# Kernel optimization log

Measured on AMD Instinct MI355X. Metric: run time of the kernel, lower is better.

## Reference

```python
import jax, jax.numpy as jnp
import numpy as np
import math

B, NTOK, NH, D = 8, 1000, 8, 64
CHUNK = 8  # query-chunk size for the pairwise L1 score computation


def _linearm(w, x):
    # LinearM: w [out, in+1] (last column is bias); x [b, t, in] -> [b, t, out]
    return jnp.einsum('oi,bti->bto', w[:, :-1], x) + w[:, -1]


def setup_inputs() -> dict:
    key = jax.random.key(0)
    ks = jax.random.split(key, 4)
    scl = 0.005
    x = jax.random.normal(ks[0], (B, NTOK, D), dtype=jnp.float32)
    wq = (scl * jax.random.normal(ks[1], (NH * D, D + 1), dtype=jnp.float32)).at[:, -1].set(0.0)
    wv = (scl * jax.random.normal(ks[2], (NH * D, D + 1), dtype=jnp.float32)).at[:, -1].set(0.0)
    wk = scl * jnp.ones((NH, D), dtype=jnp.float32)
    wf = (scl * jax.random.normal(ks[3], (D, D + 1), dtype=jnp.float32)).at[:, -1].set(0.0)
    return {"x": x, "wq": wq, "wv": wv, "wk": wk, "wf": wf}


def _forward(x, wq, wv, wk, wf):
    b, t, d = x.shape
    nh = wk.shape[0]
    scale = 1.0 / math.sqrt(d)

    q = _linearm(wq, x).reshape(b, t, nh, d)          # [b, t, nh, d]
    v = _linearm(wv, x).reshape(b, t, nh, d)          # [b, t, nh, d]
    k = x[:, :, None, :] * wk[None, None]             # [b, t, nh, d]

    # L1-distance attention scores: a[b, s, q, h] = -scale * sum_w |q[b,q,h,w] - k[b,s,h,w]|
    # Computed in query chunks so the [b, t, t, nh, d] pairwise tensor is never materialized.
    nc = t // CHUNK
    qc = q.reshape(b, nc, CHUNK, nh, d).transpose(1, 0, 2, 3, 4)  # [nc, b, C, nh, d]

    @jax.checkpoint
    def scores(qch):
        # qch: [b, C, nh, d] -> [b, t(src), C, nh]
        return -scale * jnp.sum(jnp.abs(qch[:, None] - k[:, :, None]), axis=-1)

    a = jax.lax.map(scores, qc)                       # [nc, b, t, C, nh]
    a = a.transpose(1, 2, 0, 3, 4).reshape(b, t, t, nh)  # [b, src, dst, nh]

    # Extra all-zero "null" source row (mirrors a[:, a2len, :, :] = 0 before softmax)
    a = jnp.concatenate([a, jnp.zeros((b, 1, t, nh), a.dtype)], axis=1)
    a = jax.nn.softmax(a, axis=1)[:, :t]              # softmax over sources, drop null row

    # einsum('bsdh,bshw->bdhw') followed by sum over heads, fused:
    out = jnp.einsum('bsth,bshw->btw', a, v)          # [b, t, d]

    y = jax.nn.relu(out)                              # self.gelu is actually ReLU
    y = _linearm(wf, y)
    return x + y


def reference(x, wq, wv, wk, wf):
    return _forward(x, wq, wv, wk, wf)
```

## Files before the change

kernel.cpp:

```cpp
#include <hip/hip_runtime.h>
#include <math.h>

#define Bb 8
#define Tt 1000
#define TPAD 1024
#define NHh 8
#define Dd 64

typedef short bf16x8 __attribute__((ext_vector_type(8)));
typedef float f32x4 __attribute__((ext_vector_type(4)));

#define QOFF (-0.3f)
#define QSTEP (0.6f / 256.0f)
#define QINV (256.0f / 0.6f)
#define CQ (-0.125f * 1.44269504088896341f * QSTEP)

__device__ __forceinline__ unsigned sad_u8(unsigned a, unsigned b, unsigned c) {
#if __has_builtin(__builtin_amdgcn_sad_u8)
    return __builtin_amdgcn_sad_u8(a, b, c);
#else
    unsigned d;
    asm("v_sad_u8 %0, %1, %2, %3" : "=v"(d) : "v"(a), "v"(b), "v"(c));
    return d;
#endif
}

__device__ __forceinline__ unsigned quant8(float v) {
    float t = (v - QOFF) * QINV + 0.5f;
    t = fminf(fmaxf(t, 0.0f), 255.0f);
    return (unsigned)(int)t;
}

__device__ __forceinline__ unsigned cvt_pk_bf16(float lo, float hi) {
    unsigned r;
    asm("v_cvt_pk_bf16_f32 %0, %1, %2" : "=v"(r) : "v"(lo), "v"(hi));
    return r;
}

__device__ __forceinline__ unsigned short f2bf(float v) {
    return (unsigned short)(cvt_pk_bf16(v, v) & 0xffffu);
}

__device__ __forceinline__ float bf2f(unsigned short u) {
    union { unsigned u; float f; } x; x.u = ((unsigned)u) << 16; return x.f;
}

__device__ __forceinline__ bf16x8 mkbf(unsigned u0, unsigned u1, unsigned u2, unsigned u3) {
    union { unsigned u[4]; bf16x8 v; } x;
    x.u[0] = u0; x.u[1] = u1; x.u[2] = u2; x.u[3] = u3;
    return x.v;
}

__device__ __forceinline__ bf16x8 bfc(uint4 q) {
    union { uint4 q; bf16x8 v; } x; x.q = q; return x.v;
}

#define GLDS(gsrc, ldst) \
    __builtin_amdgcn_global_load_lds((const __attribute__((address_space(1))) unsigned*)(gsrc), \
                                     (__attribute__((address_space(3))) unsigned*)(ldst), 16, 0, 0)

__global__ __launch_bounds__(256) void prep_kernel(
    const float* __restrict__ x, const float* __restrict__ wq,
    const float* __restrict__ wv, const float* __restrict__ wk,
    unsigned* __restrict__ qq8, unsigned* __restrict__ kq8,
    uint4* __restrict__ vfrag)
{
    __shared__ float xs[64][68];
    __shared__ float ws[64][65];
    __shared__ float vS[64][68];
    const int tid = threadIdx.x;
    const int st = blockIdx.x;
    const int cb = blockIdx.y;
    const int b  = blockIdx.z;
    const bool isQ = (cb < 8);
    const int h = isQ ? cb : (cb - 8);
    const float* W = isQ ? wq : wv;
    const int cBase = h * 64;
    const int bh = b * NHh + h;

#pragma unroll
    for (int i = 0; i < 4; ++i) {
        int f4 = tid + i * 256;
        int r = f4 >> 4, c4 = (f4 & 15) << 2;
        int row = st * 64 + r; if (row >= Tt) row = Tt - 1;
        *(float4*)&xs[r][c4] = *(const float4*)&x[((size_t)b * Tt + row) * 64 + c4];
    }
#pragma unroll
    for (int i = 0; i < 16; ++i) {
        int idx = tid + i * 256;
        int c = idx >> 6, k = idx & 63;
        ws[c][k] = W[(cBase + c) * 65 + k];
    }
    __syncthreads();

    const int rg = tid >> 4, cg = tid & 15;
    const int r0 = rg * 4, c0 = cg * 4;
    float acc[4][4];
#pragma unroll
    for (int j = 0; j < 4; ++j) {
        float bias = W[(cBase + c0 + j) * 65 + 64];
#pragma unroll
        for (int i = 0; i < 4; ++i) acc[i][j] = bias;
    }
    for (int k0 = 0; k0 < 64; k0 += 4) {
        float4 a[4];
#pragma unroll
        for (int i = 0; i < 4; ++i) a[i] = *(const float4*)&xs[r0 + i][k0];
#pragma unroll
        for (int j = 0; j < 4; ++j) {
            float b0 = ws[c0 + j][k0 + 0];
            float b1 = ws[c0 + j][k0 + 1];
            float b2 = ws[c0 + j][k0 + 2];
            float b3 = ws[c0 + j][k0 + 3];
#pragma unroll
            for (int i = 0; i < 4; ++i)
                acc[i][j] += a[i].x * b0 + a[i].y * b1 + a[i].z * b2 + a[i].w * b3;
        }
    }

    if (isQ) {
#pragma unroll
        for (int i = 0; i < 4; ++i) {
            int t = st * 64 + r0 + i;
            unsigned d = 0u;
            if (t < Tt)
                d = quant8(acc[i][0]) | (quant8(acc[i][1]) << 8) |
                    (quant8(acc[i][2]) << 16) | (quant8(acc[i][3]) << 24);
            qq8[((size_t)bh * TPAD + t) * 16 + cg] = d;
        }
        {
            const int r = tid >> 2, c4 = tid & 3;
            const int t = st * 64 + r;
            unsigned kd[4];
            if (t < Tt) {
#pragma unroll
                for (int dw = 0; dw < 4; ++dw) {
                    int w = c4 * 16 + dw * 4;
                    float4 wkv = *(const float4*)&wk[h * 64 + w];
                    kd[dw] = quant8(xs[r][w + 0] * wkv.x) |
                             (quant8(xs[r][w + 1] * wkv.y) << 8) |
                             (quant8(xs[r][w + 2] * wkv.z) << 16) |
                             (quant8(xs[r][w + 3] * wkv.w) << 24);
                }
            } else {
                kd[0] = kd[1] = kd[2] = kd[3] = 0u;
            }
            const int c4s = c4 ^ ((r >> 3) & 3);
            *(uint4*)&kq8[((size_t)bh * TPAD + t) * 16 + c4s * 4] =
                make_uint4(kd[0], kd[1], kd[2], kd[3]);
        }
    } else {
#pragma unroll
        for (int i = 0; i < 4; ++i) {
            float4 o; o.x = acc[i][0]; o.y = acc[i][1]; o.z = acc[i][2]; o.w = acc[i][3];
            *(float4*)&vS[r0 + i][c0] = o;
        }
        __syncthreads();
#pragma unroll
        for (int e2 = 0; e2 < 2; ++e2) {
            int ent = tid + e2 * 256;
            int kk = ent >> 8, rem = ent & 255, n = rem >> 6, lane = rem & 63;
            int ts = kk * 32 + ((lane >> 4) << 3);
            int w  = n * 16 + (lane & 15);
            unsigned o[4];
#pragma unroll
            for (int pr = 0; pr < 4; ++pr) {
                int t0 = st * 64 + ts + pr * 2;
                float lo = (t0 < Tt)     ? vS[ts + pr * 2][w]     : 0.0f;
                float hi = (t0 + 1 < Tt) ? vS[ts + pr * 2 + 1][w] : 0.0f;
                o[pr] = cvt_pk_bf16(lo, hi);
            }
            vfrag[(((size_t)bh * 16 + st) * 8 + (kk * 4 + n)) * 64 + lane] =
                make_uint4(o[0], o[1], o[2], o[3]);
        }
    }
}

__global__ __launch_bounds__(256) void attn_kernel(
    const unsigned* __restrict__ qq8, const unsigned* __restrict__ kq8,
    const uint4* __restrict__ vfrag,
    unsigned short* __restrict__ numbf, float* __restrict__ dsums)
{
    __shared__ uint4 smem[1024];
    __shared__ float dred[2][2][16];

    const int tid = threadIdx.x;
    const int wv_ = tid >> 6;
    const int l   = tid & 63;
    const int g   = l >> 4;
    const int m   = l & 15;
    const int qt  = blockIdx.x;
    const int h   = blockIdx.y;
    const int bz  = blockIdx.z;
    const int b   = bz >> 1;
    const int half = bz & 1;
    const int bh  = b * NHh + h;
    const int rowhalf = wv_ & 1;
    const int tileq   = wv_ >> 1;
    const int rowbase = qt * 64 + rowhalf * 32;
    const int tbase   = half * 8 + tileq * 4;

    unsigned qa[16], qb[16];
    {
        const uint4* qp = (const uint4*)qq8 + ((size_t)bh * TPAD + rowbase + m) * 4;
        *(uint4*)&qa[0]  = qp[0];  *(uint4*)&qa[4]  = qp[1];
        *(uint4*)&qa[8]  = qp[2];  *(uint4*)&qa[12] = qp[3];
        const uint4* qp2 = qp + 64;
        *(uint4*)&qb[0]  = qp2[0]; *(uint4*)&qb[4]  = qp2[1];
        *(uint4*)&qb[8]  = qp2[2]; *(uint4*)&qb[12] = qp2[3];
    }

    const uint4* kg = (const uint4*)kq8 + (size_t)bh * 4096;
    const uint4* vg = vfrag + (size_t)bh * 8192;

#define STAGEK(I, BUF) do { \
        GLDS(kg + (half * 8 + (I)) * 256 + wv_ * 64 + l,     &smem[(0 * 2 + (BUF)) * 256 + wv_ * 64]); \
        GLDS(kg + (half * 8 + 4 + (I)) * 256 + wv_ * 64 + l, &smem[(1 * 2 + (BUF)) * 256 + wv_ * 64]); \
    } while (0)

    STAGEK(0, 0);
    __syncthreads();

    f32x4 aca[4], acb[4];
#pragma unroll
    for (int n = 0; n < 4; ++n) { aca[n] = (f32x4){0.f,0.f,0.f,0.f}; acb[n] = aca[n]; }
    float dsum_a = 0.0f, dsum_b = 0.0f;

#pragma unroll 1
    for (int i = 0; i < 4; ++i) {
        const int cur = i & 1;
        const int t = tbase + i;
        const uint4* kbase = &smem[(tileq * 2 + cur) * 256];
        const uint4* vt = vg + (size_t)t * 512 + l;

        if (i < 3) STAGEK(i + 1, cur ^ 1);

        uint4 vf0 = vt[0 * 64], vf1 = vt[1 * 64], vf2 = vt[2 * 64], vf3 = vt[3 * 64];

        bf16x8 Aa0, Ab0;
        {
            unsigned wa[4], wb[4];
            float pva = 0.f, pvb = 0.f;
#pragma unroll
            for (int e = 0; e < 8; ++e) {
                const uint4* kb = kbase + ((g << 3) + e) * 4;
                uint4 c0 = kb[0 ^ g], c1 = kb[1 ^ g], c2 = kb[2 ^ g], c3 = kb[3 ^ g];
                const unsigned* k0 = (const unsigned*)&c0;
                const unsigned* k1 = (const unsigned*)&c1;
                const unsigned* k2 = (const unsigned*)&c2;
                const unsigned* k3 = (const unsigned*)&c3;
                unsigned sa0 = 0u, sa1 = 0u, sb0 = 0u, sb1 = 0u;
#pragma unroll
                for (int w = 0; w < 4; ++w) {
                    sa0 = sad_u8(qa[w],      k0[w], sa0);
                    sa1 = sad_u8(qa[4 + w],  k1[w], sa1);
                    sb0 = sad_u8(qb[w],      k0[w], sb0);
                    sb1 = sad_u8(qb[4 + w],  k1[w], sb1);
                }
#pragma unroll
                for (int w = 0; w < 4; ++w) {
                    sa0 = sad_u8(qa[8 + w],  k2[w], sa0);
                    sa1 = sad_u8(qa[12 + w], k3[w], sa1);
                    sb0 = sad_u8(qb[8 + w],  k2[w], sb0);
                    sb1 = sad_u8(qb[12 + w], k3[w], sb1);
                }
                float pea = __builtin_amdgcn_exp2f(CQ * (float)(sa0 + sa1));
                float peb = __builtin_amdgcn_exp2f(CQ * (float)(sb0 + sb1));
                dsum_a += pea; dsum_b += peb;
                if (e & 1) { wa[e >> 1] = cvt_pk_bf16(pva, pea); wb[e >> 1] = cvt_pk_bf16(pvb, peb); }
                else       { pva = pea; pvb = peb; }
            }
            Aa0 = mkbf(wa[0], wa[1], wa[2], wa[3]);
            Ab0 = mkbf(wb[0], wb[1], wb[2], wb[3]);
        }

        aca[0] = __builtin_amdgcn_mfma_f32_16x16x32_bf16(Aa0, bfc(vf0), aca[0], 0, 0, 0);
        acb[0] = __builtin_amdgcn_mfma_f32_16x16x32_bf16(Ab0, bfc(vf0), acb[0], 0, 0, 0);
        aca[1] = __builtin_amdgcn_mfma_f32_16x16x32_bf16(Aa0, bfc(vf1), aca[1], 0, 0, 0);
        acb[1] = __builtin_amdgcn_mfma_f32_16x16x32_bf16(Ab0, bfc(vf1), acb[1], 0, 0, 0);
        aca[2] = __builtin_amdgcn_mfma_f32_16x16x32_bf16(Aa0, bfc(vf2), aca[2], 0, 0, 0);
        acb[2] = __builtin_amdgcn_mfma_f32_16x16x32_bf16(Ab0, bfc(vf2), acb[2], 0, 0, 0);
        aca[3] = __builtin_amdgcn_mfma_f32_16x16x32_bf16(Aa0, bfc(vf3), aca[3], 0, 0, 0);
        acb[3] = __builtin_amdgcn_mfma_f32_16x16x32_bf16(Ab0, bfc(vf3), acb[3], 0, 0, 0);

        uint4 vf4 = vt[4 * 64], vf5 = vt[5 * 64], vf6 = vt[6 * 64], vf7 = vt[7 * 64];

        bf16x8 Aa1, Ab1;
        {
            const bool maskall = (t == 15) && (g >= 1);
            unsigned wa[4], wb[4];
            float pva = 0.f, pvb = 0.f;
#pragma unroll
            for (int e = 0; e < 8; ++e) {
                const uint4* kb = kbase + (32 + (g << 3) + e) * 4;
                uint4 c0 = kb[0 ^ g], c1 = kb[1 ^ g], c2 = kb[2 ^ g], c3 = kb[3 ^ g];
                const unsigned* k0 = (const unsigned*)&c0;
                const unsigned* k1 = (const unsigned*)&c1;
                const unsigned* k2 = (const unsigned*)&c2;
                const unsigned* k3 = (const unsigned*)&c3;
                unsigned sa0 = 0u, sa1 = 0u, sb0 = 0u, sb1 = 0u;
#pragma unroll
                for (int w = 0; w < 4; ++w) {
                    sa0 = sad_u8(qa[w],      k0[w], sa0);
                    sa1 = sad_u8(qa[4 + w],  k1[w], sa1);
                    sb0 = sad_u8(qb[w],      k0[w], sb0);
                    sb1 = sad_u8(qb[4 + w],  k1[w], sb1);
                }
#pragma unroll
                for (int w = 0; w < 4; ++w) {
                    sa0 = sad_u8(qa[8 + w],  k2[w], sa0);
                    sa1 = sad_u8(qa[12 + w], k3[w], sa1);
                    sb0 = sad_u8(qb[8 + w],  k2[w], sb0);
                    sb1 = sad_u8(qb[12 + w], k3[w], sb1);
                }
                float pea = maskall ? 0.0f : __builtin_amdgcn_exp2f(CQ * (float)(sa0 + sa1));
                float peb = maskall ? 0.0f : __builtin_amdgcn_exp2f(CQ * (float)(sb0 + sb1));
                dsum_a += pea; dsum_b += peb;
                if (e & 1) { wa[e >> 1] = cvt_pk_bf16(pva, pea); wb[e >> 1] = cvt_pk_bf16(pvb, peb); }
                else       { pva = pea; pvb = peb; }
            }
            Aa1 = mkbf(wa[0], wa[1], wa[2], wa[3]);
            Ab1 = mkbf(wb[0], wb[1], wb[2], wb[3]);
        }

        aca[0] = __builtin_amdgcn_mfma_f32_16x16x32_bf16(Aa1, bfc(vf4), aca[0], 0, 0, 0);
        acb[0] = __builtin_amdgcn_mfma_f32_16x16x32_bf16(Ab1, bfc(vf4), acb[0], 0, 0, 0);
        aca[1] = __builtin_amdgcn_mfma_f32_16x16x32_bf16(Aa1, bfc(vf5), aca[1], 0, 0, 0);
        acb[1] = __builtin_amdgcn_mfma_f32_16x16x32_bf16(Ab1, bfc(vf5), acb[1], 0, 0, 0);
        aca[2] = __builtin_amdgcn_mfma_f32_16x16x32_bf16(Aa1, bfc(vf6), aca[2], 0, 0, 0);
        acb[2] = __builtin_amdgcn_mfma_f32_16x16x32_bf16(Ab1, bfc(vf6), acb[2], 0, 0, 0);
        aca[3] = __builtin_amdgcn_mfma_f32_16x16x32_bf16(Aa1, bfc(vf7), aca[3], 0, 0, 0);
        acb[3] = __builtin_amdgcn_mfma_f32_16x16x32_bf16(Ab1, bfc(vf7), acb[3], 0, 0, 0);

        __syncthreads();
    }
#undef STAGEK

    dsum_a += __shfl_xor(dsum_a, 16);
    dsum_a += __shfl_xor(dsum_a, 32);
    dsum_b += __shfl_xor(dsum_b, 16);
    dsum_b += __shfl_xor(dsum_b, 32);

    f32x4* red = (f32x4*)smem;
    if (tileq == 1) {
#pragma unroll
        for (int n = 0; n < 4; ++n) {
            red[(((rowhalf * 2 + 0) * 4) + n) * 64 + l] = aca[n];
            red[(((rowhalf * 2 + 1) * 4) + n) * 64 + l] = acb[n];
        }
        if (l < 16) { dred[rowhalf][0][l] = dsum_a; dred[rowhalf][1][l] = dsum_b; }
    }
    __syncthreads();
    if (tileq == 0) {
#pragma unroll
        for (int n = 0; n < 4; ++n) {
            f32x4 ra = red[(((rowhalf * 2 + 0) * 4) + n) * 64 + l];
            f32x4 rb = red[(((rowhalf * 2 + 1) * 4) + n) * 64 + l];
#pragma unroll
            for (int j = 0; j < 4; ++j) { aca[n][j] += ra[j]; acb[n][j] += rb[j]; }
        }
        const float dta = dsum_a + dred[rowhalf][0][m];
        const float dtb = dsum_b + dred[rowhalf][1][m];

#pragma unroll
        for (int j = 0; j < 4; ++j) {
            int row_a = rowbase + g * 4 + j;
            int row_b = rowbase + 16 + g * 4 + j;
            if (row_a < Tt) {
                unsigned short* o = numbf + (((size_t)(b * Tt + row_a) * 16) + h * 2 + half) * 64 + m;
                o[0]  = f2bf(aca[0][j]);
                o[16] = f2bf(aca[1][j]);
                o[32] = f2bf(aca[2][j]);
                o[48] = f2bf(aca[3][j]);
            }
            if (row_b < Tt) {
                unsigned short* o = numbf + (((size_t)(b * Tt + row_b) * 16) + h * 2 + half) * 64 + m;
                o[0]  = f2bf(acb[0][j]);
                o[16] = f2bf(acb[1][j]);
                o[32] = f2bf(acb[2][j]);
                o[48] = f2bf(acb[3][j]);
            }
        }
        if (l < 16) {
            int ra = rowbase + m, rb = rowbase + 16 + m;
            if (ra < Tt) dsums[(((size_t)(b * Tt + ra) * 8) + h) * 2 + half] = dta;
            if (rb < Tt) dsums[(((size_t)(b * Tt + rb) * 8) + h) * 2 + half] = dtb;
        }
    }
}

__global__ __launch_bounds__(256) void finalize_kernel(
    const float* __restrict__ x, const float* __restrict__ wf,
    const unsigned short* __restrict__ numbf, const float* __restrict__ dsums,
    float* __restrict__ out)
{
    __shared__ float wfs[64][65];
    __shared__ float osh[4][64];
    const int tid = threadIdx.x;
    for (int i = tid; i < 64 * 65; i += 256) wfs[i / 65][i % 65] = wf[i];
    const int wave = tid >> 6, lane = tid & 63;
    const int token = blockIdx.x * 4 + wave;

    const float dsv = dsums[(size_t)token * 16 + (lane & 15)];
    const unsigned short* np = numbf + (size_t)token * 1024;
    float o = 0.f;
#pragma unroll
    for (int hh = 0; hh < 8; ++hh) {
        float den = 1.0f + __shfl(dsv, 2 * hh) + __shfl(dsv, 2 * hh + 1);
        float inv = 1.0f / den;
        float a0 = bf2f(np[(2 * hh) * 64 + lane]);
        float a1 = bf2f(np[(2 * hh + 1) * 64 + lane]);
        o += (a0 + a1) * inv;
    }
    o = fmaxf(o, 0.f);
    osh[wave][lane] = o;
    __syncthreads();
    float acc = wfs[lane][64];
#pragma unroll 8
    for (int w = 0; w < 64; ++w) acc += wfs[lane][w] * osh[wave][w];
    out[(size_t)token * Dd + lane] = x[(size_t)token * Dd + lane] + acc;
}

extern "C" void kernel_launch(void* const* d_in, const int* in_sizes, int n_in,
                              void* d_out, int out_size, void* d_ws, size_t ws_size,
                              hipStream_t stream)
{
    const float* x  = (const float*)d_in[0];
    const float* wq = (const float*)d_in[1];
    const float* wv = (const float*)d_in[2];
    const float* wk = (const float*)d_in[3];
    const float* wf = (const float*)d_in[4];
    float* out = (float*)d_out;

    char* base = (char*)d_ws;
    unsigned short* numbf = (unsigned short*)base;
    float*    dsums = (float*)(base + 16384000);
    unsigned* qq8   = (unsigned*)(base + 16896000);
    unsigned* kq8   = (unsigned*)(base + 16896000 + 4194304);
    uint4*    vfrag = (uint4*)(base + 16896000 + 2 * 4194304);

    prep_kernel<<<dim3(16, 16, Bb), 256, 0, stream>>>(x, wq, wv, wk, qq8, kq8, vfrag);
    attn_kernel<<<dim3(16, NHh, 2 * Bb), 256, 0, stream>>>(qq8, kq8, vfrag, numbf, dsums);
    finalize_kernel<<<2000, 256, 0, stream>>>(x, wf, numbf, dsums, out);
}
```

Before: 92.00 us.

## Split K into LDS-staged and global-read halves, loop over two k-subtiles

```diff
diff --git a/kernel.cpp b/kernel.cpp
--- a/kernel.cpp
+++ b/kernel.cpp
@@ -62,7 +62,7 @@
 __global__ __launch_bounds__(256) void prep_kernel(
     const float* __restrict__ x, const float* __restrict__ wq,
     const float* __restrict__ wv, const float* __restrict__ wk,
-    unsigned* __restrict__ qq8, unsigned* __restrict__ kq8,
+    unsigned* __restrict__ qq8, uint4* __restrict__ kq8a, uint4* __restrict__ kq8b,
     uint4* __restrict__ vfrag)
 {
     __shared__ float xs[64][68];
@@ -145,9 +145,11 @@
             } else {
                 kd[0] = kd[1] = kd[2] = kd[3] = 0u;
             }
-            const int c4s = c4 ^ ((r >> 3) & 3);
-            *(uint4*)&kq8[((size_t)bh * TPAD + t) * 16 + c4s * 4] =
-                make_uint4(kd[0], kd[1], kd[2], kd[3]);
+            uint4 v4 = make_uint4(kd[0], kd[1], kd[2], kd[3]);
+            if (c4 < 2)
+                kq8a[((size_t)bh * TPAD + t) * 2 + c4] = v4;
+            else
+                kq8b[((size_t)bh * TPAD + t) * 2 + (c4 - 2)] = v4;
         }
     } else {
 #pragma unroll
@@ -177,8 +179,8 @@
 }
 
 __global__ __launch_bounds__(256) void attn_kernel(
-    const unsigned* __restrict__ qq8, const unsigned* __restrict__ kq8,
-    const uint4* __restrict__ vfrag,
+    const unsigned* __restrict__ qq8, const uint4* __restrict__ kq8a,
+    const uint4* __restrict__ kq8b, const uint4* __restrict__ vfrag,
     unsigned short* __restrict__ numbf, float* __restrict__ dsums)
 {
     __shared__ uint4 smem[1024];
@@ -210,13 +212,19 @@
         *(uint4*)&qb[8]  = qp2[2]; *(uint4*)&qb[12] = qp2[3];
     }
 
-    const uint4* kg = (const uint4*)kq8 + (size_t)bh * 4096;
-    const uint4* vg = vfrag + (size_t)bh * 8192;
-
-#define STAGEK(I, BUF) do { \
-        GLDS(kg + (half * 8 + (I)) * 256 + wv_ * 64 + l,     &smem[(0 * 2 + (BUF)) * 256 + wv_ * 64]); \
-        GLDS(kg + (half * 8 + 4 + (I)) * 256 + wv_ * 64 + l, &smem[(1 * 2 + (BUF)) * 256 + wv_ * 64]); \
-    } while (0)
+    const unsigned* kga = (const unsigned*)kq8a + (size_t)bh * TPAD * 8;
+    const uint4*    kgb = kq8b + (size_t)bh * TPAD * 2;
+    const uint4*    vg  = vfrag + (size_t)bh * 8192;
+
+    const int hu = wv_ & 1;
+    const int st_row = hu * 32 + (((l >> 1) & 3) << 3) + (l >> 3);
+    const int st_off = st_row * 8 + (l & 1) * 4;
+
+    unsigned* kSd = (unsigned*)smem;
+
+#define STAGEK(I, BUF) \
+    GLDS(kga + ((size_t)(tbase + (I)) * 64) * 8 + st_off, \
+         kSd + (((BUF) * 2 + tileq) * 512 + hu * 256))
 
     STAGEK(0, 0);
     __syncthreads();
@@ -230,70 +238,30 @@
     for (int i = 0; i < 4; ++i) {
         const int cur = i & 1;
         const int t = tbase + i;
-        const uint4* kbase = &smem[(tileq * 2 + cur) * 256];
+        const uint4* kb = (const uint4*)(kSd + (cur * 2 + tileq) * 512);
         const uint4* vt = vg + (size_t)t * 512 + l;
 
         if (i < 3) STAGEK(i + 1, cur ^ 1);
 
-        uint4 vf0 = vt[0 * 64], vf1 = vt[1 * 64], vf2 = vt[2 * 64], vf3 = vt[3 * 64];
-
-        bf16x8 Aa0, Ab0;
-        {
+#pragma unroll
+        for (int kk = 0; kk < 2; ++kk) {
+            uint4 vf0 = vt[(kk * 4 + 0) * 64];
+            uint4 vf1 = vt[(kk * 4 + 1) * 64];
+            uint4 vf2 = vt[(kk * 4 + 2) * 64];
+            uint4 vf3 = vt[(kk * 4 + 3) * 64];
+
+            const uint4* kbl = kb + kk * 64 + g * 2;
+            const uint4* gk  = kgb + ((size_t)t * 64 + kk * 32 + (g << 3)) * 2;
+
+            const bool maskall = (t == 15) && (kk == 1) && (g >= 1);
             unsigned wa[4], wb[4];
             float pva = 0.f, pvb = 0.f;
 #pragma unroll
             for (int e = 0; e < 8; ++e) {
-                const uint4* kb = kbase + ((g << 3) + e) * 4;
-                uint4 c0 = kb[0 ^ g], c1 = kb[1 ^ g], c2 = kb[2 ^ g], c3 = kb[3 ^ g];
-                const unsigned* k0 = (const unsigned*)&c0;
-                const unsigned* k1 = (const unsigned*)&c1;
-                const unsigned* k2 = (const unsigned*)&c2;
-                const unsigned* k3 = (const unsigned*)&c3;
-                unsigned sa0 = 0u, sa1 = 0u, sb0 = 0u, sb1 = 0u;
-#pragma unroll
-                for (int w = 0; w < 4; ++w) {
-                    sa0 = sad_u8(qa[w],      k0[w], sa0);
-                    sa1 = sad_u8(qa[4 + w],  k1[w], sa1);
-                    sb0 = sad_u8(qb[w],      k0[w], sb0);
-                    sb1 = sad_u8(qb[4 + w],  k1[w], sb1);
-                }
-#pragma unroll
-                for (int w = 0; w < 4; ++w) {
-                    sa0 = sad_u8(qa[8 + w],  k2[w], sa0);
-                    sa1 = sad_u8(qa[12 + w], k3[w], sa1);
-                    sb0 = sad_u8(qb[8 + w],  k2[w], sb0);
-                    sb1 = sad_u8(qb[12 + w], k3[w], sb1);
-                }
-                float pea = __builtin_amdgcn_exp2f(CQ * (float)(sa0 + sa1));
-                float peb = __builtin_amdgcn_exp2f(CQ * (float)(sb0 + sb1));
-                dsum_a += pea; dsum_b += peb;
-                if (e & 1) { wa[e >> 1] = cvt_pk_bf16(pva, pea); wb[e >> 1] = cvt_pk_bf16(pvb, peb); }
-                else       { pva = pea; pvb = peb; }
-            }
-            Aa0 = mkbf(wa[0], wa[1], wa[2], wa[3]);
-            Ab0 = mkbf(wb[0], wb[1], wb[2], wb[3]);
-        }
-
-        aca[0] = __builtin_amdgcn_mfma_f32_16x16x32_bf16(Aa0, bfc(vf0), aca[0], 0, 0, 0);
-        acb[0] = __builtin_amdgcn_mfma_f32_16x16x32_bf16(Ab0, bfc(vf0), acb[0], 0, 0, 0);
-        aca[1] = __builtin_amdgcn_mfma_f32_16x16x32_bf16(Aa0, bfc(vf1), aca[1], 0, 0, 0);
-        acb[1] = __builtin_amdgcn_mfma_f32_16x16x32_bf16(Ab0, bfc(vf1), acb[1], 0, 0, 0);
-        aca[2] = __builtin_amdgcn_mfma_f32_16x16x32_bf16(Aa0, bfc(vf2), aca[2], 0, 0, 0);
-        acb[2] = __builtin_amdgcn_mfma_f32_16x16x32_bf16(Ab0, bfc(vf2), acb[2], 0, 0, 0);
-        aca[3] = __builtin_amdgcn_mfma_f32_16x16x32_bf16(Aa0, bfc(vf3), aca[3], 0, 0, 0);
-        acb[3] = __builtin_amdgcn_mfma_f32_16x16x32_bf16(Ab0, bfc(vf3), acb[3], 0, 0, 0);
-
-        uint4 vf4 = vt[4 * 64], vf5 = vt[5 * 64], vf6 = vt[6 * 64], vf7 = vt[7 * 64];
-
-        bf16x8 Aa1, Ab1;
-        {
-            const bool maskall = (t == 15) && (g >= 1);
-            unsigned wa[4], wb[4];
-            float pva = 0.f, pvb = 0.f;
-#pragma unroll
-            for (int e = 0; e < 8; ++e) {
-                const uint4* kb = kbase + (32 + (g << 3) + e) * 4;
-                uint4 c0 = kb[0 ^ g], c1 = kb[1 ^ g], c2 = kb[2 ^ g], c3 = kb[3 ^ g];
+                uint4 c0 = kbl[e * 8];
+                uint4 c1 = kbl[e * 8 + 1];
+                uint4 c2 = gk[e * 2];
+                uint4 c3 = gk[e * 2 + 1];
                 const unsigned* k0 = (const unsigned*)&c0;
                 const unsigned* k1 = (const unsigned*)&c1;
                 const unsigned* k2 = (const unsigned*)&c2;
@@ -319,18 +287,18 @@
                 if (e & 1) { wa[e >> 1] = cvt_pk_bf16(pva, pea); wb[e >> 1] = cvt_pk_bf16(pvb, peb); }
                 else       { pva = pea; pvb = peb; }
             }
-            Aa1 = mkbf(wa[0], wa[1], wa[2], wa[3]);
-            Ab1 = mkbf(wb[0], wb[1], wb[2], wb[3]);
-        }
-
-        aca[0] = __builtin_amdgcn_mfma_f32_16x16x32_bf16(Aa1, bfc(vf4), aca[0], 0, 0, 0);
-        acb[0] = __builtin_amdgcn_mfma_f32_16x16x32_bf16(Ab1, bfc(vf4), acb[0], 0, 0, 0);
-        aca[1] = __builtin_amdgcn_mfma_f32_16x16x32_bf16(Aa1, bfc(vf5), aca[1], 0, 0, 0);
-        acb[1] = __builtin_amdgcn_mfma_f32_16x16x32_bf16(Ab1, bfc(vf5), acb[1], 0, 0, 0);
-        aca[2] = __builtin_amdgcn_mfma_f32_16x16x32_bf16(Aa1, bfc(vf6), aca[2], 0, 0, 0);
-        acb[2] = __builtin_amdgcn_mfma_f32_16x16x32_bf16(Ab1, bfc(vf6), acb[2], 0, 0, 0);
-        aca[3] = __builtin_amdgcn_mfma_f32_16x16x32_bf16(Aa1, bfc(vf7), aca[3], 0, 0, 0);
-        acb[3] = __builtin_amdgcn_mfma_f32_16x16x32_bf16(Ab1, bfc(vf7), acb[3], 0, 0, 0);
+            bf16x8 Aa = mkbf(wa[0], wa[1], wa[2], wa[3]);
+            bf16x8 Ab = mkbf(wb[0], wb[1], wb[2], wb[3]);
+
+            aca[0] = __builtin_amdgcn_mfma_f32_16x16x32_bf16(Aa, bfc(vf0), aca[0], 0, 0, 0);
+            acb[0] = __builtin_amdgcn_mfma_f32_16x16x32_bf16(Ab, bfc(vf0), acb[0], 0, 0, 0);
+            aca[1] = __builtin_amdgcn_mfma_f32_16x16x32_bf16(Aa, bfc(vf1), aca[1], 0, 0, 0);
+            acb[1] = __builtin_amdgcn_mfma_f32_16x16x32_bf16(Ab, bfc(vf1), acb[1], 0, 0, 0);
+            aca[2] = __builtin_amdgcn_mfma_f32_16x16x32_bf16(Aa, bfc(vf2), aca[2], 0, 0, 0);
+            acb[2] = __builtin_amdgcn_mfma_f32_16x16x32_bf16(Ab, bfc(vf2), acb[2], 0, 0, 0);
+            aca[3] = __builtin_amdgcn_mfma_f32_16x16x32_bf16(Aa, bfc(vf3), aca[3], 0, 0, 0);
+            acb[3] = __builtin_amdgcn_mfma_f32_16x16x32_bf16(Ab, bfc(vf3), acb[3], 0, 0, 0);
+        }
 
         __syncthreads();
     }
@@ -436,10 +404,11 @@
     unsigned short* numbf = (unsigned short*)base;
     float*    dsums = (float*)(base + 16384000);
     unsigned* qq8   = (unsigned*)(base + 16896000);
-    unsigned* kq8   = (unsigned*)(base + 16896000 + 4194304);
+    uint4*    kq8a  = (uint4*)(base + 16896000 + 4194304);
+    uint4*    kq8b  = (uint4*)(base + 16896000 + 4194304 + 2097152);
     uint4*    vfrag = (uint4*)(base + 16896000 + 2 * 4194304);
 
-    prep_kernel<<<dim3(16, 16, Bb), 256, 0, stream>>>(x, wq, wv, wk, qq8, kq8, vfrag);
-    attn_kernel<<<dim3(16, NHh, 2 * Bb), 256, 0, stream>>>(qq8, kq8, vfrag, numbf, dsums);
+    prep_kernel<<<dim3(16, 16, Bb), 256, 0, stream>>>(x, wq, wv, wk, qq8, kq8a, kq8b, vfrag);
+    attn_kernel<<<dim3(16, NHh, 2 * Bb), 256, 0, stream>>>(qq8, kq8a, kq8b, vfrag, numbf, dsums);
     finalize_kernel<<<2000, 256, 0, stream>>>(x, wf, numbf, dsums, out);
 }
```

New measurement: 97.90 us. 6.4% more time.

## Use bf16 MFMA for Q/V projection and transpose numerator layout for vector loads

Applied to the files above, without the earlier changes.

```diff
diff --git a/kernel.cpp b/kernel.cpp
--- a/kernel.cpp
+++ b/kernel.cpp
@@ -55,19 +55,18 @@
     union { uint4 q; bf16x8 v; } x; x.q = q; return x.v;
 }
 
-#define GLDS(gsrc, ldst) \
-    __builtin_amdgcn_global_load_lds((const __attribute__((address_space(1))) unsigned*)(gsrc), \
-                                     (__attribute__((address_space(3))) unsigned*)(ldst), 16, 0, 0)
-
 __global__ __launch_bounds__(256) void prep_kernel(
     const float* __restrict__ x, const float* __restrict__ wq,
     const float* __restrict__ wv, const float* __restrict__ wk,
     unsigned* __restrict__ qq8, unsigned* __restrict__ kq8,
     uint4* __restrict__ vfrag)
 {
-    __shared__ float xs[64][68];
-    __shared__ float ws[64][65];
+    __shared__ unsigned short xsb[64][72];
+    __shared__ unsigned short wsb[64][72];
+    __shared__ float biasS[64];
+    __shared__ float wkS[64];
     __shared__ float vS[64][68];
+
     const int tid = threadIdx.x;
     const int st = blockIdx.x;
     const int cb = blockIdx.y;
@@ -83,50 +82,53 @@
         int f4 = tid + i * 256;
         int r = f4 >> 4, c4 = (f4 & 15) << 2;
         int row = st * 64 + r; if (row >= Tt) row = Tt - 1;
-        *(float4*)&xs[r][c4] = *(const float4*)&x[((size_t)b * Tt + row) * 64 + c4];
+        float4 v = *(const float4*)&x[((size_t)b * Tt + row) * 64 + c4];
+        unsigned d0 = cvt_pk_bf16(v.x, v.y);
+        unsigned d1 = cvt_pk_bf16(v.z, v.w);
+        *(uint2*)&xsb[r][c4] = make_uint2(d0, d1);
     }
 #pragma unroll
     for (int i = 0; i < 16; ++i) {
         int idx = tid + i * 256;
         int c = idx >> 6, k = idx & 63;
-        ws[c][k] = W[(cBase + c) * 65 + k];
+        wsb[c][k] = f2bf(W[(cBase + c) * 65 + k]);
+    }
+    if (tid < 64) {
+        biasS[tid] = W[(cBase + tid) * 65 + 64];
+        wkS[tid]   = wk[h * 64 + tid];
     }
     __syncthreads();
 
-    const int rg = tid >> 4, cg = tid & 15;
-    const int r0 = rg * 4, c0 = cg * 4;
-    float acc[4][4];
-#pragma unroll
-    for (int j = 0; j < 4; ++j) {
-        float bias = W[(cBase + c0 + j) * 65 + 64];
-#pragma unroll
-        for (int i = 0; i < 4; ++i) acc[i][j] = bias;
-    }
-    for (int k0 = 0; k0 < 64; k0 += 4) {
-        float4 a[4];
-#pragma unroll
-        for (int i = 0; i < 4; ++i) a[i] = *(const float4*)&xs[r0 + i][k0];
+    const int rb = tid >> 6, l = tid & 63;
+    const int m = l & 15, g = l >> 4;
+
+    f32x4 acc[4];
+#pragma unroll
+    for (int n = 0; n < 4; ++n) {
+        float bv = biasS[16 * n + m];
+        acc[n] = (f32x4){bv, bv, bv, bv};
+    }
+    {
+        bf16x8 xa0 = *(const bf16x8*)&xsb[16 * rb + m][g * 8];
+        bf16x8 xa1 = *(const bf16x8*)&xsb[16 * rb + m][32 + g * 8];
+#pragma unroll
+        for (int n = 0; n < 4; ++n) {
+            bf16x8 wb0 = *(const bf16x8*)&wsb[16 * n + m][g * 8];
+            bf16x8 wb1 = *(const bf16x8*)&wsb[16 * n + m][32 + g * 8];
+            acc[n] = __builtin_amdgcn_mfma_f32_16x16x32_bf16(xa0, wb0, acc[n], 0, 0, 0);
+            acc[n] = __builtin_amdgcn_mfma_f32_16x16x32_bf16(xa1, wb1, acc[n], 0, 0, 0);
+        }
+    }
+
+    if (isQ) {
 #pragma unroll
         for (int j = 0; j < 4; ++j) {
-            float b0 = ws[c0 + j][k0 + 0];
-            float b1 = ws[c0 + j][k0 + 1];
-            float b2 = ws[c0 + j][k0 + 2];
-            float b3 = ws[c0 + j][k0 + 3];
-#pragma unroll
-            for (int i = 0; i < 4; ++i)
-                acc[i][j] += a[i].x * b0 + a[i].y * b1 + a[i].z * b2 + a[i].w * b3;
-        }
-    }
-
-    if (isQ) {
-#pragma unroll
-        for (int i = 0; i < 4; ++i) {
-            int t = st * 64 + r0 + i;
+            int t = st * 64 + 16 * rb + g * 4 + j;
             unsigned d = 0u;
             if (t < Tt)
-                d = quant8(acc[i][0]) | (quant8(acc[i][1]) << 8) |
-                    (quant8(acc[i][2]) << 16) | (quant8(acc[i][3]) << 24);
-            qq8[((size_t)bh * TPAD + t) * 16 + cg] = d;
+                d = quant8(acc[0][j]) | (quant8(acc[1][j]) << 8) |
+                    (quant8(acc[2][j]) << 16) | (quant8(acc[3][j]) << 24);
+            qq8[((size_t)bh * TPAD + (t < Tt ? t : st * 64 + 16 * rb + g * 4 + j)) * 16 + m] = d;
         }
         {
             const int r = tid >> 2, c4 = tid & 3;
@@ -135,12 +137,13 @@
             if (t < Tt) {
 #pragma unroll
                 for (int dw = 0; dw < 4; ++dw) {
-                    int w = c4 * 16 + dw * 4;
-                    float4 wkv = *(const float4*)&wk[h * 64 + w];
-                    kd[dw] = quant8(xs[r][w + 0] * wkv.x) |
-                             (quant8(xs[r][w + 1] * wkv.y) << 8) |
-                             (quant8(xs[r][w + 2] * wkv.z) << 16) |
-                             (quant8(xs[r][w + 3] * wkv.w) << 24);
+                    int wbase = 4 * c4 + dw;
+                    float e0 = bf2f(xsb[r][wbase])      * wkS[wbase];
+                    float e1 = bf2f(xsb[r][wbase + 16]) * wkS[wbase + 16];
+                    float e2 = bf2f(xsb[r][wbase + 32]) * wkS[wbase + 32];
+                    float e3 = bf2f(xsb[r][wbase + 48]) * wkS[wbase + 48];
+                    kd[dw] = quant8(e0) | (quant8(e1) << 8) |
+                             (quant8(e2) << 16) | (quant8(e3) << 24);
                 }
             } else {
                 kd[0] = kd[1] = kd[2] = kd[3] = 0u;
@@ -151,9 +154,10 @@
         }
     } else {
 #pragma unroll
-        for (int i = 0; i < 4; ++i) {
-            float4 o; o.x = acc[i][0]; o.y = acc[i][1]; o.z = acc[i][2]; o.w = acc[i][3];
-            *(float4*)&vS[r0 + i][c0] = o;
+        for (int j = 0; j < 4; ++j) {
+            int row = 16 * rb + g * 4 + j;
+#pragma unroll
+            for (int n = 0; n < 4; ++n) vS[row][m + 16 * n] = acc[n][j];
         }
         __syncthreads();
 #pragma unroll
@@ -213,9 +217,12 @@
     const uint4* kg = (const uint4*)kq8 + (size_t)bh * 4096;
     const uint4* vg = vfrag + (size_t)bh * 8192;
 
+#define GLDS(gsrc, ldst) \
+    __builtin_amdgcn_global_load_lds((const __attribute__((address_space(1))) unsigned*)(gsrc), \
+                                     (__attribute__((address_space(3))) unsigned*)(ldst), 16, 0, 0)
 #define STAGEK(I, BUF) do { \
-        GLDS(kg + (half * 8 + (I)) * 256 + wv_ * 64 + l,     &smem[(0 * 2 + (BUF)) * 256 + wv_ * 64]); \
-        GLDS(kg + (half * 8 + 4 + (I)) * 256 + wv_ * 64 + l, &smem[(1 * 2 + (BUF)) * 256 + wv_ * 64]); \
+        GLDS(kg + (half * 8 + (I)) * 256 + wv_ * 64 + l,     &((unsigned*)smem)[((0 * 2 + (BUF)) * 256 + wv_ * 64) * 4]); \
+        GLDS(kg + (half * 8 + 4 + (I)) * 256 + wv_ * 64 + l, &((unsigned*)smem)[((1 * 2 + (BUF)) * 256 + wv_ * 64) * 4]); \
     } while (0)
 
     STAGEK(0, 0);
@@ -335,6 +342,7 @@
         __syncthreads();
     }
 #undef STAGEK
+#undef GLDS
 
     dsum_a += __shfl_xor(dsum_a, 16);
     dsum_a += __shfl_xor(dsum_a, 32);
@@ -367,18 +375,18 @@
             int row_a = rowbase + g * 4 + j;
             int row_b = rowbase + 16 + g * 4 + j;
             if (row_a < Tt) {
-                unsigned short* o = numbf + (((size_t)(b * Tt + row_a) * 16) + h * 2 + half) * 64 + m;
-                o[0]  = f2bf(aca[0][j]);
-                o[16] = f2bf(aca[1][j]);
-                o[32] = f2bf(aca[2][j]);
-                o[48] = f2bf(aca[3][j]);
+                unsigned short* o = numbf + (((size_t)(b * Tt + row_a) * 64 + m) * 16) + h * 2 + half;
+                o[0]   = f2bf(aca[0][j]);
+                o[256] = f2bf(aca[1][j]);
+                o[512] = f2bf(aca[2][j]);
+                o[768] = f2bf(aca[3][j]);
             }
             if (row_b < Tt) {
-                unsigned short* o = numbf + (((size_t)(b * Tt + row_b) * 16) + h * 2 + half) * 64 + m;
-                o[0]  = f2bf(acb[0][j]);
-                o[16] = f2bf(acb[1][j]);
-                o[32] = f2bf(acb[2][j]);
-                o[48] = f2bf(acb[3][j]);
+                unsigned short* o = numbf + (((size_t)(b * Tt + row_b) * 64 + m) * 16) + h * 2 + half;
+                o[0]   = f2bf(acb[0][j]);
+                o[256] = f2bf(acb[1][j]);
+                o[512] = f2bf(acb[2][j]);
+                o[768] = f2bf(acb[3][j]);
             }
         }
         if (l < 16) {
@@ -402,14 +410,17 @@
     const int token = blockIdx.x * 4 + wave;
 
     const float dsv = dsums[(size_t)token * 16 + (lane & 15)];
-    const unsigned short* np = numbf + (size_t)token * 1024;
+    const unsigned* np = (const unsigned*)(numbf + ((size_t)token * 64 + lane) * 16);
+    uint4 u0 = *(const uint4*)np;
+    uint4 u1 = *(const uint4*)(np + 4);
+    unsigned uu[8] = {u0.x, u0.y, u0.z, u0.w, u1.x, u1.y, u1.z, u1.w};
     float o = 0.f;
 #pragma unroll
     for (int hh = 0; hh < 8; ++hh) {
         float den = 1.0f + __shfl(dsv, 2 * hh) + __shfl(dsv, 2 * hh + 1);
         float inv = 1.0f / den;
-        float a0 = bf2f(np[(2 * hh) * 64 + lane]);
-        float a1 = bf2f(np[(2 * hh + 1) * 64 + lane]);
+        float a0 = bf2f((unsigned short)(uu[hh] & 0xffffu));
+        float a1 = bf2f((unsigned short)(uu[hh] >> 16));
         o += (a0 + a1) * inv;
     }
     o = fmaxf(o, 0.f);
```

After: 94.06 us. +2.2%, slower.
